# Kernel tuning notes

Hardware: AMD Instinct MI355X
Metric: run time of the kernel (lower is better)

Reference implementation:

```python
import jax, jax.numpy as jnp
import numpy as np

H, KVH, D, HID = 32, 32, 128, 4096
THETA = 10000.0
EPS = 1e-5


def setup_inputs() -> dict:
    key = jax.random.key(0)
    ks = jax.random.split(key, 7)
    T = 2048
    return {
        "positions": jnp.arange(T, dtype=jnp.int32),
        "hidden_states": jax.random.normal(ks[0], (T, HID), dtype=jnp.float32),
        "w_qkv": jax.random.normal(ks[1], ((H + 2 * KVH) * D, HID), dtype=jnp.float32) * 0.02,
        "w_o": jax.random.normal(ks[2], (HID, H * D), dtype=jnp.float32) * 0.02,
        "q_norm_w": jax.random.uniform(ks[3], (H, D), dtype=jnp.float32),
        "q_norm_b": jax.random.normal(ks[4], (H, D), dtype=jnp.float32) * 0.02,
        "k_norm_w": jax.random.uniform(ks[5], (KVH, D), dtype=jnp.float32),
        "k_norm_b": jax.random.normal(ks[6], (KVH, D), dtype=jnp.float32) * 0.02,
    }


def _per_head_ln(x, w, b):
    # x: [T, H, D]; layer_norm over last dim without affine, then *w + b (per head)
    mu = jnp.mean(x, axis=-1, keepdims=True)
    var = jnp.mean(jnp.square(x - mu), axis=-1, keepdims=True)
    xn = (x - mu) * jax.lax.rsqrt(var + EPS)
    return xn * w + b


def _rope(x, positions):
    # neox-style rotate-half RoPE; x: [T, H, D]
    half = D // 2
    inv_freq = 1.0 / (THETA ** (jnp.arange(0, D, 2, dtype=jnp.float32) / D))  # [D/2]
    freqs = positions.astype(jnp.float32)[:, None] * inv_freq  # [T, D/2]
    cos = jnp.cos(freqs)[:, None, :]  # [T, 1, D/2]
    sin = jnp.sin(freqs)[:, None, :]
    x1, x2 = x[..., :half], x[..., half:]
    return jnp.concatenate([x1 * cos - x2 * sin, x2 * cos + x1 * sin], axis=-1)


def reference(positions, hidden_states, w_qkv, w_o, q_norm_w, q_norm_b, k_norm_w, k_norm_b):
    T = hidden_states.shape[0]
    qkv = hidden_states @ w_qkv.T  # [T, (H+2*KVH)*D]
    q, k, v = jnp.split(qkv, [H * D, (H + KVH) * D], axis=-1)
    q = q.reshape(T, H, D)
    k = k.reshape(T, KVH, D)
    v = v.reshape(T, KVH, D)
    q = _per_head_ln(q, q_norm_w, q_norm_b)
    k = _per_head_ln(k, k_norm_w, k_norm_b)
    q = _rope(q, positions)
    k = _rope(k, positions)
    scale = D ** -0.5
    scores = jnp.einsum("qhd,khd->hqk", q, k) * scale  # [H, T, T]
    causal = jnp.tril(jnp.ones((T, T), dtype=bool))
    scores = jnp.where(causal, scores, jnp.finfo(scores.dtype).min)
    probs = jax.nn.softmax(scores, axis=-1)
    attn = jnp.einsum("hqk,khd->qhd", probs, v).reshape(T, H * D)
    return attn @ w_o.T  # [T, HID]
```

## Files before the change

### kernel.cpp

```cpp
#include <hip/hip_runtime.h>
#include <cstdint>

typedef unsigned short u16;
typedef __attribute__((ext_vector_type(8))) __bf16 bf16x8;
typedef __attribute__((ext_vector_type(4))) float f32x4;

__device__ __forceinline__ u16 f2bf(float f) {
  unsigned int u = __builtin_bit_cast(unsigned int, f);
  unsigned int r = (u + 0x7fffu + ((u >> 16) & 1u)) >> 16;
  return (u16)r;
}
__device__ __forceinline__ float bf2f(u16 u) {
  return __builtin_bit_cast(float, (unsigned int)u << 16);
}

__device__ __forceinline__ void gload16(const u16* g, u16* l) {
  __builtin_amdgcn_global_load_lds((const __attribute__((address_space(1))) void*)g,
                                   (__attribute__((address_space(3))) void*)l, 16, 0, 0);
}

__device__ __forceinline__ int swz64i(int row, int col) {
  return row * 64 + (((col & 0x38) ^ ((row & 7) << 3)) | (col & 7));
}
__device__ __forceinline__ int swz128i(int row, int col) {
  return row * 128 + (((col & 0x78) ^ ((row & 7) << 3)) | (col & 7));
}

__global__ __launch_bounds__(256) void cvt_bf16_kernel(const float* __restrict__ in,
                                                       u16* __restrict__ out, long n4) {
  long i = (long)blockIdx.x * 256 + threadIdx.x;
  long stride = (long)gridDim.x * 256;
  const float4* in4 = (const float4*)in;
  uint2* out2 = (uint2*)out;
  for (long k = i; k < n4; k += stride) {
    float4 v = in4[k];
    uint2 o;
    o.x = (unsigned int)f2bf(v.x) | ((unsigned int)f2bf(v.y) << 16);
    o.y = (unsigned int)f2bf(v.z) | ((unsigned int)f2bf(v.w) << 16);
    out2[k] = o;
  }
}

__global__ __launch_bounds__(512, 2) void gemm192(const u16* __restrict__ A,
                                                  const u16* __restrict__ B,
                                                  u16* __restrict__ C,
                                                  int Ndim, int Kdim) {
  extern __shared__ __align__(16) u16 lds[];
  const int tid = threadIdx.x;
  const int lane = tid & 63, wave = tid >> 6;
  const int wr = wave >> 2, wc = wave & 3;
  const int l15 = lane & 15, l4 = lane >> 4;
  const int gx = gridDim.x;
  int lin = blockIdx.y * gx + blockIdx.x;
  const int xcd = lin & 7, ii = lin >> 3;
  const int bx = xcd * (gx >> 3) + (ii >> 3), by = ii & 7;
  const long arow = (long)by * 256, brow = (long)bx * 192;
  const int NT = Kdim >> 6;

  const int rowt = tid >> 3;
  const int koff = ((tid & 7) ^ (rowt & 7)) * 8;
  const u16* gA[4];
  const u16* gB[3];
  #pragma unroll
  for (int r = 0; r < 4; ++r) gA[r] = A + (size_t)(arow + rowt + r * 64) * Kdim + koff;
  #pragma unroll
  for (int r = 0; r < 3; ++r) gB[r] = B + (size_t)(brow + rowt + r * 64) * Kdim + koff;
  u16* const ldsB = lds + 49152;

  auto STA = [&](int u) {
    u16* d = lds + (u % 3) * 16384 + tid * 8;
    #pragma unroll
    for (int r = 0; r < 4; ++r) gload16(gA[r] + (size_t)u * 64, d + r * 4096);
  };
  auto STB = [&](int u) {
    u16* d = ldsB + (u & 1) * 12288 + tid * 8;
    #pragma unroll
    for (int r = 0; r < 3; ++r) gload16(gB[r] + (size_t)u * 64, d + r * 4096);
  };

  bf16x8 af[4][2], bfr[3][2];
  f32x4 acc[8][3] = {};
  int cks[2];
  #pragma unroll
  for (int kc = 0; kc < 2; ++kc) cks[kc] = (((kc * 4 + l4) ^ (l15 & 7)) * 8);

  auto LDA4 = [&](int u, int mh) {
    const u16* base = lds + (u % 3) * 16384 + (wr * 128 + mh * 64 + l15) * 64;
    #pragma unroll
    for (int m = 0; m < 4; ++m)
      #pragma unroll
      for (int kc = 0; kc < 2; ++kc)
        af[m][kc] = *(const bf16x8*)(base + m * 1024 + cks[kc]);
  };
  auto LDBall = [&](int u) {
    const u16* base = ldsB + (u & 1) * 12288 + (wc * 48 + l15) * 64;
    #pragma unroll
    for (int nh = 0; nh < 3; ++nh)
      #pragma unroll
      for (int kc = 0; kc < 2; ++kc)
        bfr[nh][kc] = *(const bf16x8*)(base + nh * 1024 + cks[kc]);
  };
  auto MM24 = [&](int mh) {
    #pragma unroll
    for (int kc = 0; kc < 2; ++kc)
      #pragma unroll
      for (int m = 0; m < 4; ++m)
        #pragma unroll
        for (int nh = 0; nh < 3; ++nh)
          acc[mh * 4 + m][nh] = __builtin_amdgcn_mfma_f32_16x16x32_bf16(
              af[m][kc], bfr[nh][kc], acc[mh * 4 + m][nh], 0, 0, 0);
  };

#define PH_BEGIN() do { __builtin_amdgcn_s_barrier();                         \
    asm volatile("s_waitcnt lgkmcnt(0)" ::: "memory");                        \
    __builtin_amdgcn_sched_barrier(0);                                        \
    __builtin_amdgcn_s_setprio(1); } while (0)
#define PH_END() do { __builtin_amdgcn_s_setprio(0);                          \
    __builtin_amdgcn_s_barrier(); } while (0)

  STA(0); STB(0); STA(1);
  asm volatile("s_waitcnt vmcnt(4)" ::: "memory");
  __builtin_amdgcn_s_barrier();

  for (int u = 0; u < NT; ++u) {
    LDA4(u, 0); LDBall(u);
    if (u + 1 < NT) STB(u + 1);
    PH_BEGIN(); MM24(0); PH_END();
    LDA4(u, 1);
    if (u + 2 < NT) STA(u + 2);
    PH_BEGIN(); MM24(1);
    __builtin_amdgcn_s_setprio(0);
    if (u + 2 < NT) { asm volatile("s_waitcnt vmcnt(4)" ::: "memory"); }
    else            { asm volatile("s_waitcnt vmcnt(0)" ::: "memory"); }
    __builtin_amdgcn_s_barrier();
  }
#undef PH_BEGIN
#undef PH_END

  #pragma unroll
  for (int m = 0; m < 8; ++m)
    #pragma unroll
    for (int nh = 0; nh < 3; ++nh)
      #pragma unroll
      for (int j = 0; j < 4; ++j) {
        long r = arow + wr * 128 + m * 16 + l4 * 4 + j;
        long c = brow + wc * 48 + nh * 16 + l15;
        C[r * Ndim + c] = f2bf(acc[m][nh][j]);
      }
}

__global__ __launch_bounds__(512, 2) void gemm256(const u16* __restrict__ A,
                                                  const u16* __restrict__ B,
                                                  float* __restrict__ C,
                                                  int Ndim, int Kdim) {
  extern __shared__ __align__(16) u16 lds[];
  const int tid = threadIdx.x;
  const int lane = tid & 63, wave = tid >> 6;
  const int wr = wave >> 2, wc = wave & 3;
  const int l15 = lane & 15, l4 = lane >> 4;
  const int gx = gridDim.x;
  int lin = blockIdx.y * gx + blockIdx.x;
  const int xcd = lin & 7, ii = lin >> 3;
  const int bx = xcd * (gx >> 3) + (ii >> 3), by = ii & 7;
  const long arow = (long)by * 256, brow = (long)bx * 128;
  const int NT = Kdim >> 6;

  const int rowt = tid >> 3;
  const int koff = ((tid & 7) ^ (rowt & 7)) * 8;
  const u16* gA[4];
  const u16* gB[2];
  #pragma unroll
  for (int r = 0; r < 4; ++r) gA[r] = A + (size_t)(arow + rowt + r * 64) * Kdim + koff;
  #pragma unroll
  for (int r = 0; r < 2; ++r) gB[r] = B + (size_t)(brow + rowt + r * 64) * Kdim + koff;

  auto STA = [&](int u) {
    u16* d = lds + (u % 3) * 16384 + tid * 8;
    #pragma unroll
    for (int r = 0; r < 4; ++r) gload16(gA[r] + (size_t)u * 64, d + r * 4096);
  };
  auto STB = [&](int u) {
    u16* d = lds + 49152 + (u & 1) * 8192 + tid * 8;
    #pragma unroll
    for (int r = 0; r < 2; ++r) gload16(gB[r] + (size_t)u * 64, d + r * 4096);
  };

  bf16x8 af[4][2], bfr[2][2];
  f32x4 acc[8][2] = {};
  int cks[2];
  #pragma unroll
  for (int kc = 0; kc < 2; ++kc) cks[kc] = (((kc * 4 + l4) ^ (l15 & 7)) * 8);

  auto LDA = [&](int u, int mh) {
    const u16* base = lds + (u % 3) * 16384 + (wr * 128 + mh * 64 + l15) * 64;
    #pragma unroll
    for (int m = 0; m < 4; ++m)
      #pragma unroll
      for (int kc = 0; kc < 2; ++kc)
        af[m][kc] = *(const bf16x8*)(base + m * 1024 + cks[kc]);
  };
  auto LDB = [&](int u) {
    const u16* base = lds + 49152 + (u & 1) * 8192 + (wc * 32 + l15) * 64;
    #pragma unroll
    for (int n = 0; n < 2; ++n)
      #pragma unroll
      for (int kc = 0; kc < 2; ++kc)
        bfr[n][kc] = *(const bf16x8*)(base + n * 1024 + cks[kc]);
  };
  auto MM = [&](int mh) {
    #pragma unroll
    for (int kc = 0; kc < 2; ++kc)
      #pragma unroll
      for (int m = 0; m < 4; ++m)
        #pragma unroll
        for (int n = 0; n < 2; ++n)
          acc[mh * 4 + m][n] =
            __builtin_amdgcn_mfma_f32_16x16x32_bf16(af[m][kc], bfr[n][kc],
                                                    acc[mh * 4 + m][n], 0, 0, 0);
  };

#define PH_BEGIN() do { __builtin_amdgcn_s_barrier();                         \
    asm volatile("s_waitcnt lgkmcnt(0)" ::: "memory");                        \
    __builtin_amdgcn_sched_barrier(0);                                        \
    __builtin_amdgcn_s_setprio(1); } while (0)

  STA(0); STB(0); STA(1); STB(1);
  asm volatile("s_waitcnt vmcnt(6)" ::: "memory");
  __builtin_amdgcn_s_barrier();

  for (int u = 0; u < NT; ++u) {
    LDA(u, 0); LDB(u);
    if (u + 2 < NT) STA(u + 2);
    PH_BEGIN(); MM(0);
    __builtin_amdgcn_s_setprio(0);
    __builtin_amdgcn_s_barrier();
    LDA(u, 1);
    if (u + 2 < NT) STB(u + 2);
    PH_BEGIN(); MM(1);
    __builtin_amdgcn_s_setprio(0);
    if (u + 2 < NT) { asm volatile("s_waitcnt vmcnt(6)" ::: "memory"); }
    else if (u + 1 < NT) { asm volatile("s_waitcnt vmcnt(0)" ::: "memory"); }
    __builtin_amdgcn_s_barrier();
  }
#undef PH_BEGIN

  #pragma unroll
  for (int M = 0; M < 8; ++M)
    #pragma unroll
    for (int n = 0; n < 2; ++n)
      #pragma unroll
      for (int j = 0; j < 4; ++j) {
        long r = arow + wr * 128 + M * 16 + l4 * 4 + j;
        long c = brow + wc * 32 + n * 16 + l15;
        C[r * Ndim + c] = acc[M][n][j];
      }
}

__global__ __launch_bounds__(256) void ln_rope_kernel(
    const u16* __restrict__ qkv, const int* __restrict__ pos,
    const float* __restrict__ qw, const float* __restrict__ qb2,
    const float* __restrict__ kw, const float* __restrict__ kb2,
    u16* __restrict__ qo, u16* __restrict__ ko, u16* __restrict__ vo, int T) {
  const int hh = blockIdx.x;
  const int t = blockIdx.y * 4 + (threadIdx.x >> 6);
  const int lane = threadIdx.x & 63;
  const u16* src = qkv + (size_t)t * 12288 + hh * 128;
  u16 u1 = src[lane], u2 = src[lane + 64];
  if (hh >= 64) {
    u16* dst = vo + ((size_t)(hh - 64) * T + t) * 128;
    dst[lane] = u1; dst[lane + 64] = u2;
    return;
  }
  float x1 = bf2f(u1), x2 = bf2f(u2);
  float s = x1 + x2;
  #pragma unroll
  for (int off = 32; off; off >>= 1) s += __shfl_xor(s, off);
  float mu = s * (1.0f / 128.0f);
  float d1 = x1 - mu, d2 = x2 - mu;
  float vs = d1 * d1 + d2 * d2;
  #pragma unroll
  for (int off = 32; off; off >>= 1) vs += __shfl_xor(vs, off);
  float rstd = rsqrtf(vs * (1.0f / 128.0f) + 1e-5f);
  bool isq = hh < 32;
  int hl = isq ? hh : hh - 32;
  const float* w = (isq ? qw : kw) + hl * 128;
  const float* b = (isq ? qb2 : kb2) + hl * 128;
  float y1 = d1 * rstd * w[lane] + b[lane];
  float y2 = d2 * rstd * w[lane + 64] + b[lane + 64];
  float p = (float)pos[t];
  float invf = exp2f((float)lane * (-13.287712379549449f / 64.0f));
  float fr = p * invf;
  float sn, cs;
  __sincosf(fr, &sn, &cs);
  float o1 = y1 * cs - y2 * sn;
  float o2 = y2 * cs + y1 * sn;
  if (isq) {
    const float sc = 0.08838834764831845f;
    o1 *= sc; o2 *= sc;
    u16* dst = qo + ((size_t)hl * T + t) * 128;
    dst[lane] = f2bf(o1); dst[lane + 64] = f2bf(o2);
  } else {
    u16* dst = ko + ((size_t)hl * T + t) * 128;
    dst[lane] = f2bf(o1); dst[lane + 64] = f2bf(o2);
  }
}

__global__ __launch_bounds__(512, 2) void flash_kernel(
    const u16* __restrict__ qb, const u16* __restrict__ kb,
    const u16* __restrict__ vb, u16* __restrict__ attn, int T) {
  extern __shared__ __align__(16) u16 flds[];
  u16* const Ks = flds;
  u16* const Vt = flds + 8192;
  u16* const Ps = flds + 16384;
  const int tid = threadIdx.x;
  const int lane = tid & 63, wave = tid >> 6;
  const int wl = wave & 3;
  const int l15 = lane & 15, l4 = lane >> 4;
  const int h = blockIdx.y;
  const int nqt = T >> 7;
  const int qt = (wave < 4) ? (nqt - 1 - blockIdx.x) : blockIdx.x;
  const int qbase = qt * 128;
  const u16* Q  = qb + (size_t)h * T * 128;
  const u16* Kp = kb + (size_t)h * T * 128;
  const u16* Vp = vb + (size_t)h * T * 128;
  const int rK = tid >> 4, d8k = (tid & 15) * 8;
  const int rv = tid & 63, dv0 = (tid >> 6) * 8;
  u16* const Pw = Ps + wave * 2048;

  bf16x8 qf[2][4];
  #pragma unroll
  for (int mi = 0; mi < 2; ++mi)
    #pragma unroll
    for (int kc = 0; kc < 4; ++kc)
      qf[mi][kc] = *(const bf16x8*)&Q[(size_t)(qbase + mi * 64 + wl * 16 + l15) * 128 + kc * 32 + l4 * 8];

  float m_st[2][4], l_st[2][4];
  f32x4 o[2][8] = {};
  #pragma unroll
  for (int mi = 0; mi < 2; ++mi)
    #pragma unroll
    for (int j = 0; j < 4; ++j) { m_st[mi][j] = -1e30f; l_st[mi][j] = 0.0f; }

  const int ntile = 2 * (nqt - 1 - blockIdx.x) + 2;
  uint4 kr[2], vr[2];
  #pragma unroll
  for (int c = 0; c < 2; ++c) {
    kr[c] = *(const uint4*)&Kp[(size_t)(rK + 32 * c) * 128 + d8k];
    vr[c] = *(const uint4*)&Vp[(size_t)rv * 128 + dv0 + 64 * c];
  }
  for (int kt = 0; kt < ntile; ++kt) {
    const int kbase = kt * 64;
    #pragma unroll
    for (int c = 0; c < 2; ++c) {
      *(uint4*)&Ks[swz128i(rK + 32 * c, d8k)] = kr[c];
      const u16* pv = (const u16*)&vr[c];
      #pragma unroll
      for (int j = 0; j < 8; ++j) Vt[swz64i(dv0 + 64 * c + j, rv)] = pv[j];
    }
    __syncthreads();
    if (kt + 1 < ntile) {
      const int nb = kbase + 64;
      #pragma unroll
      for (int c = 0; c < 2; ++c) {
        kr[c] = *(const uint4*)&Kp[(size_t)(nb + rK + 32 * c) * 128 + d8k];
        vr[c] = *(const uint4*)&Vp[(size_t)(nb + rv) * 128 + dv0 + 64 * c];
      }
    }
    #pragma unroll
    for (int mi = 0; mi < 2; ++mi) {
      const int r0 = qbase + mi * 64 + wl * 16;
      if (kbase <= r0 + 15) {
        f32x4 s[4] = {};
        __builtin_amdgcn_s_setprio(1);
        #pragma unroll
        for (int kc = 0; kc < 4; ++kc)
          #pragma unroll
          for (int nj = 0; nj < 4; ++nj) {
            bf16x8 kf = *(const bf16x8*)&Ks[swz128i(nj * 16 + l15, kc * 32 + l4 * 8)];
            s[nj] = __builtin_amdgcn_mfma_f32_16x16x32_bf16(qf[mi][kc], kf, s[nj], 0, 0, 0);
          }
        __builtin_amdgcn_s_setprio(0);
        if (kbase + 63 > r0) {
          #pragma unroll
          for (int nj = 0; nj < 4; ++nj)
            #pragma unroll
            for (int j = 0; j < 4; ++j) {
              int r = r0 + l4 * 4 + j;
              int cc = kbase + nj * 16 + l15;
              if (cc > r) s[nj][j] = -1e30f;
            }
        }
        float vmax[4];
        float dmax = -1e30f;
        #pragma unroll
        for (int j = 0; j < 4; ++j) {
          float v = fmaxf(fmaxf(s[0][j], s[1][j]), fmaxf(s[2][j], s[3][j]));
          #pragma unroll
          for (int off = 1; off < 16; off <<= 1) v = fmaxf(v, __shfl_xor(v, off));
          vmax[j] = v;
          dmax = fmaxf(dmax, v - m_st[mi][j]);
        }
        if (!__all(dmax <= 8.0f)) {
          #pragma unroll
          for (int j = 0; j < 4; ++j) {
            float mn = fmaxf(m_st[mi][j], vmax[j]);
            float scl = __expf(m_st[mi][j] - mn);
            m_st[mi][j] = mn;
            l_st[mi][j] *= scl;
            #pragma unroll
            for (int nf = 0; nf < 8; ++nf) o[mi][nf][j] *= scl;
          }
        }
        float sum[4] = {0.f, 0.f, 0.f, 0.f};
        #pragma unroll
        for (int nj = 0; nj < 4; ++nj)
          #pragma unroll
          for (int j = 0; j < 4; ++j) {
            float p = __expf(s[nj][j] - m_st[mi][j]);
            s[nj][j] = p;
            sum[j] += p;
          }
        #pragma unroll
        for (int j = 0; j < 4; ++j) {
          #pragma unroll
          for (int off = 1; off < 16; off <<= 1) sum[j] += __shfl_xor(sum[j], off);
          l_st[mi][j] += sum[j];
        }
        #pragma unroll
        for (int nj = 0; nj < 4; ++nj)
          #pragma unroll
          for (int j = 0; j < 4; ++j)
            Pw[swz64i(mi * 16 + l4 * 4 + j, nj * 16 + l15)] = f2bf(s[nj][j]);
        asm volatile("s_waitcnt lgkmcnt(0)" ::: "memory");
        __builtin_amdgcn_sched_barrier(0);
        __builtin_amdgcn_s_setprio(1);
        #pragma unroll
        for (int kc = 0; kc < 2; ++kc) {
          bf16x8 pf = *(const bf16x8*)&Pw[swz64i(mi * 16 + l15, kc * 32 + l4 * 8)];
          #pragma unroll
          for (int nf = 0; nf < 8; ++nf) {
            bf16x8 vf = *(const bf16x8*)&Vt[swz64i(nf * 16 + l15, kc * 32 + l4 * 8)];
            o[mi][nf] = __builtin_amdgcn_mfma_f32_16x16x32_bf16(pf, vf, o[mi][nf], 0, 0, 0);
          }
        }
        __builtin_amdgcn_s_setprio(0);
      }
    }
    __syncthreads();
  }
  #pragma unroll
  for (int mi = 0; mi < 2; ++mi) {
    float rl[4];
    #pragma unroll
    for (int j = 0; j < 4; ++j) rl[j] = 1.0f / l_st[mi][j];
    #pragma unroll
    for (int nf = 0; nf < 8; ++nf)
      #pragma unroll
      for (int j = 0; j < 4; ++j) {
        int r = qbase + mi * 64 + wl * 16 + l4 * 4 + j;
        int cc = h * 128 + nf * 16 + l15;
        attn[(size_t)r * 4096 + cc] = f2bf(o[mi][nf][j] * rl[j]);
      }
  }
}

extern "C" void kernel_launch(void* const* d_in, const int* in_sizes, int n_in,
                              void* d_out, int out_size, void* d_ws, size_t ws_size,
                              hipStream_t stream) {
  const int* positions = (const int*)d_in[0];
  const float* hidden  = (const float*)d_in[1];
  const float* w_qkv   = (const float*)d_in[2];
  const float* w_o     = (const float*)d_in[3];
  const float* qnw     = (const float*)d_in[4];
  const float* qnb     = (const float*)d_in[5];
  const float* knw     = (const float*)d_in[6];
  const float* knb     = (const float*)d_in[7];
  float* out = (float*)d_out;

  const int T = in_sizes[0];
  const int HID = 4096, NQKV = 12288, H = 32;

  char* ws = (char*)d_ws;
  u16* hid_bf  = (u16*)ws;
  u16* wreg    = (u16*)(ws + (size_t)T * HID * 2);
  u16* qkv_bf  = (u16*)(ws + (size_t)T * HID * 2 + (size_t)NQKV * HID * 2);

  u16* q_bf  = wreg;
  u16* k_bf  = q_bf + (size_t)H * T * 128;
  u16* v_bf  = k_bf + (size_t)H * T * 128;
  u16* at_bf = v_bf + (size_t)H * T * 128;
  u16* wo_bf = at_bf + (size_t)T * 4096;

  hipFuncSetAttribute(reinterpret_cast<const void*>(&gemm192),
                      hipFuncAttributeMaxDynamicSharedMemorySize, 147456);
  hipFuncSetAttribute(reinterpret_cast<const void*>(&gemm256),
                      hipFuncAttributeMaxDynamicSharedMemorySize, 131072);
  hipFuncSetAttribute(reinterpret_cast<const void*>(&flash_kernel),
                      hipFuncAttributeMaxDynamicSharedMemorySize, 65536);

  cvt_bf16_kernel<<<2048, 256, 0, stream>>>(hidden, hid_bf, (long)T * HID / 4);
  cvt_bf16_kernel<<<4096, 256, 0, stream>>>(w_qkv, wreg, (long)NQKV * HID / 4);
  gemm192<<<dim3(NQKV / 192, T / 256), 512, 147456, stream>>>(hid_bf, wreg, qkv_bf, NQKV, HID);
  ln_rope_kernel<<<dim3(96, T / 4), 256, 0, stream>>>(qkv_bf, positions, qnw, qnb, knw, knb,
                                                      q_bf, k_bf, v_bf, T);
  cvt_bf16_kernel<<<2048, 256, 0, stream>>>(w_o, wo_bf, (long)HID * HID / 4);
  flash_kernel<<<dim3(T / 256, H), 512, 65536, stream>>>(q_bf, k_bf, v_bf, at_bf, T);
  gemm256<<<dim3(HID / 128, T / 256), 512, 131072, stream>>>(at_bf, wo_bf, out, HID, HID);
}
```

Before: 498.6 us.

## Fuse fp32 weight conversion into GEMM B-tile loads

New measurement: 547.5 us. 9.8% more time.

```diff
diff --git a/kernel.cpp b/kernel.cpp
--- a/kernel.cpp
+++ b/kernel.cpp
@@ -12,6 +12,12 @@
 }
 __device__ __forceinline__ float bf2f(u16 u) {
   return __builtin_bit_cast(float, (unsigned int)u << 16);
+}
+__device__ __forceinline__ bf16x8 pack8(float4 a, float4 b) {
+  bf16x8 r;
+  r[0] = (__bf16)a.x; r[1] = (__bf16)a.y; r[2] = (__bf16)a.z; r[3] = (__bf16)a.w;
+  r[4] = (__bf16)b.x; r[5] = (__bf16)b.y; r[6] = (__bf16)b.z; r[7] = (__bf16)b.w;
+  return r;
 }
 
 __device__ __forceinline__ void gload16(const u16* g, u16* l) {
@@ -42,7 +48,7 @@
 }
 
 __global__ __launch_bounds__(512, 2) void gemm192(const u16* __restrict__ A,
-                                                  const u16* __restrict__ B,
+                                                  const float* __restrict__ W,
                                                   u16* __restrict__ C,
                                                   int Ndim, int Kdim) {
   extern __shared__ __align__(16) u16 lds[];
@@ -60,11 +66,11 @@
   const int rowt = tid >> 3;
   const int koff = ((tid & 7) ^ (rowt & 7)) * 8;
   const u16* gA[4];
-  const u16* gB[3];
+  const float* gW[3];
   #pragma unroll
   for (int r = 0; r < 4; ++r) gA[r] = A + (size_t)(arow + rowt + r * 64) * Kdim + koff;
   #pragma unroll
-  for (int r = 0; r < 3; ++r) gB[r] = B + (size_t)(brow + rowt + r * 64) * Kdim + koff;
+  for (int r = 0; r < 3; ++r) gW[r] = W + (size_t)(brow + rowt + r * 64) * Kdim + koff;
   u16* const ldsB = lds + 49152;
 
   auto STA = [&](int u) {
@@ -72,10 +78,19 @@
     #pragma unroll
     for (int r = 0; r < 4; ++r) gload16(gA[r] + (size_t)u * 64, d + r * 4096);
   };
-  auto STB = [&](int u) {
+  float4 breg[3][2];
+  auto GLB = [&](int u) {
+    #pragma unroll
+    for (int r = 0; r < 3; ++r) {
+      breg[r][0] = *(const float4*)(gW[r] + (size_t)u * 64);
+      breg[r][1] = *(const float4*)(gW[r] + (size_t)u * 64 + 4);
+    }
+  };
+  auto CVW = [&](int u) {
     u16* d = ldsB + (u & 1) * 12288 + tid * 8;
     #pragma unroll
-    for (int r = 0; r < 3; ++r) gload16(gB[r] + (size_t)u * 64, d + r * 4096);
+    for (int r = 0; r < 3; ++r)
+      *(bf16x8*)(d + r * 4096) = pack8(breg[r][0], breg[r][1]);
   };
 
   bf16x8 af[4][2], bfr[3][2];
@@ -118,20 +133,27 @@
 #define PH_END() do { __builtin_amdgcn_s_setprio(0);                          \
     __builtin_amdgcn_s_barrier(); } while (0)
 
-  STA(0); STB(0); STA(1);
+  GLB(0);
+  __builtin_amdgcn_sched_barrier(0);
+  STA(0); STA(1);
+  asm volatile("s_waitcnt vmcnt(8)" ::: "memory");
+  CVW(0);
   asm volatile("s_waitcnt vmcnt(4)" ::: "memory");
+  asm volatile("s_waitcnt lgkmcnt(0)" ::: "memory");
   __builtin_amdgcn_s_barrier();
 
   for (int u = 0; u < NT; ++u) {
     LDA4(u, 0); LDBall(u);
-    if (u + 1 < NT) STB(u + 1);
+    if (u + 1 < NT) GLB(u + 1);
+    __builtin_amdgcn_sched_barrier(0);
+    if (u + 2 < NT) STA(u + 2);
     PH_BEGIN(); MM24(0); PH_END();
     LDA4(u, 1);
-    if (u + 2 < NT) STA(u + 2);
+    if (u + 2 < NT) { asm volatile("s_waitcnt vmcnt(4)" ::: "memory"); }
+    else            { asm volatile("s_waitcnt vmcnt(0)" ::: "memory"); }
+    if (u + 1 < NT) CVW(u + 1);
     PH_BEGIN(); MM24(1);
     __builtin_amdgcn_s_setprio(0);
-    if (u + 2 < NT) { asm volatile("s_waitcnt vmcnt(4)" ::: "memory"); }
-    else            { asm volatile("s_waitcnt vmcnt(0)" ::: "memory"); }
     __builtin_amdgcn_s_barrier();
   }
 #undef PH_BEGIN
@@ -150,7 +172,7 @@
 }
 
 __global__ __launch_bounds__(512, 2) void gemm256(const u16* __restrict__ A,
-                                                  const u16* __restrict__ B,
+                                                  const float* __restrict__ W,
                                                   float* __restrict__ C,
                                                   int Ndim, int Kdim) {
   extern __shared__ __align__(16) u16 lds[];
@@ -168,21 +190,30 @@
   const int rowt = tid >> 3;
   const int koff = ((tid & 7) ^ (rowt & 7)) * 8;
   const u16* gA[4];
-  const u16* gB[2];
+  const float* gW[2];
   #pragma unroll
   for (int r = 0; r < 4; ++r) gA[r] = A + (size_t)(arow + rowt + r * 64) * Kdim + koff;
   #pragma unroll
-  for (int r = 0; r < 2; ++r) gB[r] = B + (size_t)(brow + rowt + r * 64) * Kdim + koff;
+  for (int r = 0; r < 2; ++r) gW[r] = W + (size_t)(brow + rowt + r * 64) * Kdim + koff;
 
   auto STA = [&](int u) {
     u16* d = lds + (u % 3) * 16384 + tid * 8;
     #pragma unroll
     for (int r = 0; r < 4; ++r) gload16(gA[r] + (size_t)u * 64, d + r * 4096);
   };
-  auto STB = [&](int u) {
+  float4 breg[2][2];
+  auto GLB = [&](int u) {
+    #pragma unroll
+    for (int r = 0; r < 2; ++r) {
+      breg[r][0] = *(const float4*)(gW[r] + (size_t)u * 64);
+      breg[r][1] = *(const float4*)(gW[r] + (size_t)u * 64 + 4);
+    }
+  };
+  auto CVW = [&](int u) {
     u16* d = lds + 49152 + (u & 1) * 8192 + tid * 8;
     #pragma unroll
-    for (int r = 0; r < 2; ++r) gload16(gB[r] + (size_t)u * 64, d + r * 4096);
+    for (int r = 0; r < 2; ++r)
+      *(bf16x8*)(d + r * 4096) = pack8(breg[r][0], breg[r][1]);
   };
 
   bf16x8 af[4][2], bfr[2][2];
@@ -224,22 +255,37 @@
     __builtin_amdgcn_sched_barrier(0);                                        \
     __builtin_amdgcn_s_setprio(1); } while (0)
 
-  STA(0); STB(0); STA(1); STB(1);
-  asm volatile("s_waitcnt vmcnt(6)" ::: "memory");
+  GLB(0);
+  __builtin_amdgcn_sched_barrier(0);
+  STA(0); STA(1);
+  asm volatile("s_waitcnt vmcnt(8)" ::: "memory");
+  CVW(0);
+  GLB(1);
+  asm volatile("s_waitcnt vmcnt(8)" ::: "memory");
+  CVW(1);
+  asm volatile("s_waitcnt vmcnt(4)" ::: "memory");
+  asm volatile("s_waitcnt lgkmcnt(0)" ::: "memory");
   __builtin_amdgcn_s_barrier();
 
   for (int u = 0; u < NT; ++u) {
     LDA(u, 0); LDB(u);
-    if (u + 2 < NT) STA(u + 2);
+    if (u + 2 < NT) {
+      GLB(u + 2);
+      __builtin_amdgcn_sched_barrier(0);
+      STA(u + 2);
+    }
     PH_BEGIN(); MM(0);
     __builtin_amdgcn_s_setprio(0);
     __builtin_amdgcn_s_barrier();
     LDA(u, 1);
-    if (u + 2 < NT) STB(u + 2);
+    if (u + 2 < NT) {
+      asm volatile("s_waitcnt vmcnt(4)" ::: "memory");
+      CVW(u + 2);
+    } else if (u + 1 < NT) {
+      asm volatile("s_waitcnt vmcnt(0)" ::: "memory");
+    }
     PH_BEGIN(); MM(1);
     __builtin_amdgcn_s_setprio(0);
-    if (u + 2 < NT) { asm volatile("s_waitcnt vmcnt(6)" ::: "memory"); }
-    else if (u + 1 < NT) { asm volatile("s_waitcnt vmcnt(0)" ::: "memory"); }
     __builtin_amdgcn_s_barrier();
   }
 #undef PH_BEGIN
@@ -489,7 +535,6 @@
   u16* k_bf  = q_bf + (size_t)H * T * 128;
   u16* v_bf  = k_bf + (size_t)H * T * 128;
   u16* at_bf = v_bf + (size_t)H * T * 128;
-  u16* wo_bf = at_bf + (size_t)T * 4096;
 
   hipFuncSetAttribute(reinterpret_cast<const void*>(&gemm192),
                       hipFuncAttributeMaxDynamicSharedMemorySize, 147456);
@@ -499,11 +544,9 @@
                       hipFuncAttributeMaxDynamicSharedMemorySize, 65536);
 
   cvt_bf16_kernel<<<2048, 256, 0, stream>>>(hidden, hid_bf, (long)T * HID / 4);
-  cvt_bf16_kernel<<<4096, 256, 0, stream>>>(w_qkv, wreg, (long)NQKV * HID / 4);
-  gemm192<<<dim3(NQKV / 192, T / 256), 512, 147456, stream>>>(hid_bf, wreg, qkv_bf, NQKV, HID);
+  gemm192<<<dim3(NQKV / 192, T / 256), 512, 147456, stream>>>(hid_bf, w_qkv, qkv_bf, NQKV, HID);
   ln_rope_kernel<<<dim3(96, T / 4), 256, 0, stream>>>(qkv_bf, positions, qnw, qnb, knw, knb,
                                                       q_bf, k_bf, v_bf, T);
-  cvt_bf16_kernel<<<2048, 256, 0, stream>>>(w_o, wo_bf, (long)HID * HID / 4);
   flash_kernel<<<dim3(T / 256, H), 512, 65536, stream>>>(q_bf, k_bf, v_bf, at_bf, T);
-  gemm256<<<dim3(HID / 128, T / 256), 512, 131072, stream>>>(at_bf, wo_bf, out, HID, HID);
-}
+  gemm256<<<dim3(HID / 128, T / 256), 512, 131072, stream>>>(at_bf, w_o, out, HID, HID);
+}
```

## Restructure flash attention to one 128-row query tile per block, longest-first

Applied to the files above, without the earlier changes.

After: 493.9 us. No clear change (-1.0%).

```diff
diff --git a/kernel.cpp b/kernel.cpp
--- a/kernel.cpp
+++ b/kernel.cpp
@@ -262,45 +262,50 @@
     const float* __restrict__ kw, const float* __restrict__ kb2,
     u16* __restrict__ qo, u16* __restrict__ ko, u16* __restrict__ vo, int T) {
   const int hh = blockIdx.x;
-  const int t = blockIdx.y * 4 + (threadIdx.x >> 6);
+  const int t0 = blockIdx.y * 16 + (threadIdx.x >> 6) * 4;
   const int lane = threadIdx.x & 63;
-  const u16* src = qkv + (size_t)t * 12288 + hh * 128;
-  u16 u1 = src[lane], u2 = src[lane + 64];
   if (hh >= 64) {
-    u16* dst = vo + ((size_t)(hh - 64) * T + t) * 128;
-    dst[lane] = u1; dst[lane + 64] = u2;
+    #pragma unroll
+    for (int i = 0; i < 4; ++i) {
+      int t = t0 + i;
+      const u16* src = qkv + (size_t)t * 12288 + hh * 128;
+      u16* dst = vo + ((size_t)(hh - 64) * T + t) * 128;
+      dst[lane] = src[lane];
+      dst[lane + 64] = src[lane + 64];
+    }
     return;
   }
-  float x1 = bf2f(u1), x2 = bf2f(u2);
-  float s = x1 + x2;
-  #pragma unroll
-  for (int off = 32; off; off >>= 1) s += __shfl_xor(s, off);
-  float mu = s * (1.0f / 128.0f);
-  float d1 = x1 - mu, d2 = x2 - mu;
-  float vs = d1 * d1 + d2 * d2;
-  #pragma unroll
-  for (int off = 32; off; off >>= 1) vs += __shfl_xor(vs, off);
-  float rstd = rsqrtf(vs * (1.0f / 128.0f) + 1e-5f);
   bool isq = hh < 32;
   int hl = isq ? hh : hh - 32;
-  const float* w = (isq ? qw : kw) + hl * 128;
-  const float* b = (isq ? qb2 : kb2) + hl * 128;
-  float y1 = d1 * rstd * w[lane] + b[lane];
-  float y2 = d2 * rstd * w[lane + 64] + b[lane + 64];
-  float p = (float)pos[t];
+  const float* wp = (isq ? qw : kw) + hl * 128;
+  const float* bp = (isq ? qb2 : kb2) + hl * 128;
+  float w1 = wp[lane], w2 = wp[lane + 64];
+  float b1 = bp[lane], b2 = bp[lane + 64];
   float invf = exp2f((float)lane * (-13.287712379549449f / 64.0f));
-  float fr = p * invf;
-  float sn, cs;
-  __sincosf(fr, &sn, &cs);
-  float o1 = y1 * cs - y2 * sn;
-  float o2 = y2 * cs + y1 * sn;
-  if (isq) {
-    const float sc = 0.08838834764831845f;
-    o1 *= sc; o2 *= sc;
-    u16* dst = qo + ((size_t)hl * T + t) * 128;
-    dst[lane] = f2bf(o1); dst[lane + 64] = f2bf(o2);
-  } else {
-    u16* dst = ko + ((size_t)hl * T + t) * 128;
+  u16* obase = (isq ? qo : ko) + (size_t)hl * T * 128;
+  const float sc = isq ? 0.08838834764831845f : 1.0f;
+  #pragma unroll
+  for (int i = 0; i < 4; ++i) {
+    int t = t0 + i;
+    const u16* src = qkv + (size_t)t * 12288 + hh * 128;
+    float x1 = bf2f(src[lane]), x2 = bf2f(src[lane + 64]);
+    float s = x1 + x2;
+    #pragma unroll
+    for (int off = 32; off; off >>= 1) s += __shfl_xor(s, off);
+    float mu = s * (1.0f / 128.0f);
+    float d1 = x1 - mu, d2 = x2 - mu;
+    float vs = d1 * d1 + d2 * d2;
+    #pragma unroll
+    for (int off = 32; off; off >>= 1) vs += __shfl_xor(vs, off);
+    float rstd = rsqrtf(vs * (1.0f / 128.0f) + 1e-5f);
+    float y1 = d1 * rstd * w1 + b1;
+    float y2 = d2 * rstd * w2 + b2;
+    float fr = (float)pos[t] * invf;
+    float sn, cs;
+    __sincosf(fr, &sn, &cs);
+    float o1 = (y1 * cs - y2 * sn) * sc;
+    float o2 = (y2 * cs + y1 * sn) * sc;
+    u16* dst = obase + (size_t)t * 128;
     dst[lane] = f2bf(o1); dst[lane + 64] = f2bf(o2);
   }
 }
@@ -314,34 +319,31 @@
   u16* const Ps = flds + 16384;
   const int tid = threadIdx.x;
   const int lane = tid & 63, wave = tid >> 6;
-  const int wl = wave & 3;
   const int l15 = lane & 15, l4 = lane >> 4;
-  const int h = blockIdx.y;
+  const int bid = blockIdx.x;
   const int nqt = T >> 7;
-  const int qt = (wave < 4) ? (nqt - 1 - blockIdx.x) : blockIdx.x;
+  const int h = bid & 31;
+  const int qt = (bid < 256) ? (nqt - 1 - (bid >> 5)) : ((bid - 256) >> 5);
   const int qbase = qt * 128;
   const u16* Q  = qb + (size_t)h * T * 128;
   const u16* Kp = kb + (size_t)h * T * 128;
   const u16* Vp = vb + (size_t)h * T * 128;
   const int rK = tid >> 4, d8k = (tid & 15) * 8;
   const int rv = tid & 63, dv0 = (tid >> 6) * 8;
-  u16* const Pw = Ps + wave * 2048;
-
-  bf16x8 qf[2][4];
-  #pragma unroll
-  for (int mi = 0; mi < 2; ++mi)
-    #pragma unroll
-    for (int kc = 0; kc < 4; ++kc)
-      qf[mi][kc] = *(const bf16x8*)&Q[(size_t)(qbase + mi * 64 + wl * 16 + l15) * 128 + kc * 32 + l4 * 8];
-
-  float m_st[2][4], l_st[2][4];
-  f32x4 o[2][8] = {};
-  #pragma unroll
-  for (int mi = 0; mi < 2; ++mi)
-    #pragma unroll
-    for (int j = 0; j < 4; ++j) { m_st[mi][j] = -1e30f; l_st[mi][j] = 0.0f; }
-
-  const int ntile = 2 * (nqt - 1 - blockIdx.x) + 2;
+  u16* const Pw = Ps + wave * 1024;
+
+  const int r0g = qbase + wave * 16;
+  bf16x8 qf[4];
+  #pragma unroll
+  for (int kc = 0; kc < 4; ++kc)
+    qf[kc] = *(const bf16x8*)&Q[(size_t)(r0g + l15) * 128 + kc * 32 + l4 * 8];
+
+  float m_st[4], l_st[4];
+  f32x4 o[8] = {};
+  #pragma unroll
+  for (int j = 0; j < 4; ++j) { m_st[j] = -1e30f; l_st[j] = 0.0f; }
+
+  const int ntile = 2 * qt + 2;
   uint4 kr[2], vr[2];
   #pragma unroll
   for (int c = 0; c < 2; ++c) {
@@ -366,102 +368,95 @@
         vr[c] = *(const uint4*)&Vp[(size_t)(nb + rv) * 128 + dv0 + 64 * c];
       }
     }
-    #pragma unroll
-    for (int mi = 0; mi < 2; ++mi) {
-      const int r0 = qbase + mi * 64 + wl * 16;
-      if (kbase <= r0 + 15) {
-        f32x4 s[4] = {};
-        __builtin_amdgcn_s_setprio(1);
-        #pragma unroll
-        for (int kc = 0; kc < 4; ++kc)
-          #pragma unroll
-          for (int nj = 0; nj < 4; ++nj) {
-            bf16x8 kf = *(const bf16x8*)&Ks[swz128i(nj * 16 + l15, kc * 32 + l4 * 8)];
-            s[nj] = __builtin_amdgcn_mfma_f32_16x16x32_bf16(qf[mi][kc], kf, s[nj], 0, 0, 0);
-          }
-        __builtin_amdgcn_s_setprio(0);
-        if (kbase + 63 > r0) {
-          #pragma unroll
-          for (int nj = 0; nj < 4; ++nj)
-            #pragma unroll
-            for (int j = 0; j < 4; ++j) {
-              int r = r0 + l4 * 4 + j;
-              int cc = kbase + nj * 16 + l15;
-              if (cc > r) s[nj][j] = -1e30f;
-            }
+    if (kbase <= r0g + 15) {
+      f32x4 s[4] = {};
+      __builtin_amdgcn_s_setprio(1);
+      #pragma unroll
+      for (int kc = 0; kc < 4; ++kc)
+        #pragma unroll
+        for (int nj = 0; nj < 4; ++nj) {
+          bf16x8 kf = *(const bf16x8*)&Ks[swz128i(nj * 16 + l15, kc * 32 + l4 * 8)];
+          s[nj] = __builtin_amdgcn_mfma_f32_16x16x32_bf16(qf[kc], kf, s[nj], 0, 0, 0);
         }
-        float vmax[4];
-        float dmax = -1e30f;
-        #pragma unroll
-        for (int j = 0; j < 4; ++j) {
-          float v = fmaxf(fmaxf(s[0][j], s[1][j]), fmaxf(s[2][j], s[3][j]));
-          #pragma unroll
-          for (int off = 1; off < 16; off <<= 1) v = fmaxf(v, __shfl_xor(v, off));
-          vmax[j] = v;
-          dmax = fmaxf(dmax, v - m_st[mi][j]);
-        }
-        if (!__all(dmax <= 8.0f)) {
-          #pragma unroll
-          for (int j = 0; j < 4; ++j) {
-            float mn = fmaxf(m_st[mi][j], vmax[j]);
-            float scl = __expf(m_st[mi][j] - mn);
-            m_st[mi][j] = mn;
-            l_st[mi][j] *= scl;
-            #pragma unroll
-            for (int nf = 0; nf < 8; ++nf) o[mi][nf][j] *= scl;
-          }
-        }
-        float sum[4] = {0.f, 0.f, 0.f, 0.f};
+      __builtin_amdgcn_s_setprio(0);
+      if (kbase + 63 > r0g) {
         #pragma unroll
         for (int nj = 0; nj < 4; ++nj)
           #pragma unroll
           for (int j = 0; j < 4; ++j) {
-            float p = __expf(s[nj][j] - m_st[mi][j]);
-            s[nj][j] = p;
-            sum[j] += p;
+            int r = r0g + l4 * 4 + j;
+            int cc = kbase + nj * 16 + l15;
+            if (cc > r) s[nj][j] = -1e30f;
           }
+      }
+      float vmax[4];
+      float dmax = -1e30f;
+      #pragma unroll
+      for (int j = 0; j < 4; ++j) {
+        float v = fmaxf(fmaxf(s[0][j], s[1][j]), fmaxf(s[2][j], s[3][j]));
+        #pragma unroll
+        for (int off = 1; off < 16; off <<= 1) v = fmaxf(v, __shfl_xor(v, off));
+        vmax[j] = v;
+        dmax = fmaxf(dmax, v - m_st[j]);
+      }
+      if (!__all(dmax <= 8.0f)) {
         #pragma unroll
         for (int j = 0; j < 4; ++j) {
+          float mn = fmaxf(m_st[j], vmax[j]);
+          float scl = __expf(m_st[j] - mn);
+          m_st[j] = mn;
+          l_st[j] *= scl;
           #pragma unroll
-          for (int off = 1; off < 16; off <<= 1) sum[j] += __shfl_xor(sum[j], off);
-          l_st[mi][j] += sum[j];
+          for (int nf = 0; nf < 8; ++nf) o[nf][j] *= scl;
         }
-        #pragma unroll
-        for (int nj = 0; nj < 4; ++nj)
-          #pragma unroll
-          for (int j = 0; j < 4; ++j)
-            Pw[swz64i(mi * 16 + l4 * 4 + j, nj * 16 + l15)] = f2bf(s[nj][j]);
-        asm volatile("s_waitcnt lgkmcnt(0)" ::: "memory");
-        __builtin_amdgcn_sched_barrier(0);
-        __builtin_amdgcn_s_setprio(1);
-        #pragma unroll
-        for (int kc = 0; kc < 2; ++kc) {
-          bf16x8 pf = *(const bf16x8*)&Pw[swz64i(mi * 16 + l15, kc * 32 + l4 * 8)];
-          #pragma unroll
-          for (int nf = 0; nf < 8; ++nf) {
-            bf16x8 vf = *(const bf16x8*)&Vt[swz64i(nf * 16 + l15, kc * 32 + l4 * 8)];
-            o[mi][nf] = __builtin_amdgcn_mfma_f32_16x16x32_bf16(pf, vf, o[mi][nf], 0, 0, 0);
-          }
+      }
+      float sum[4] = {0.f, 0.f, 0.f, 0.f};
+      #pragma unroll
+      for (int nj = 0; nj < 4; ++nj)
+        #pragma unroll
+        for (int j = 0; j < 4; ++j) {
+          float p = __expf(s[nj][j] - m_st[j]);
+          s[nj][j] = p;
+          sum[j] += p;
         }
-        __builtin_amdgcn_s_setprio(0);
-      }
+      #pragma unroll
+      for (int j = 0; j < 4; ++j) {
+        #pragma unroll
+        for (int off = 1; off < 16; off <<= 1) sum[j] += __shfl_xor(sum[j], off);
+        l_st[j] += sum[j];
+      }
+      #pragma unroll
+      for (int nj = 0; nj < 4; ++nj)
+        #pragma unroll
+        for (int j = 0; j < 4; ++j)
+          Pw[swz64i(l4 * 4 + j, nj * 16 + l15)] = f2bf(s[nj][j]);
+      asm volatile("s_waitcnt lgkmcnt(0)" ::: "memory");
+      __builtin_amdgcn_sched_barrier(0);
+      __builtin_amdgcn_s_setprio(1);
+      #pragma unroll
+      for (int kc = 0; kc < 2; ++kc) {
+        bf16x8 pf = *(const bf16x8*)&Pw[swz64i(l15, kc * 32 + l4 * 8)];
+        #pragma unroll
+        for (int nf = 0; nf < 8; ++nf) {
+          bf16x8 vf = *(const bf16x8*)&Vt[swz64i(nf * 16 + l15, kc * 32 + l4 * 8)];
+          o[nf] = __builtin_amdgcn_mfma_f32_16x16x32_bf16(pf, vf, o[nf], 0, 0, 0);
+        }
+      }
+      __builtin_amdgcn_s_setprio(0);
     }
     __syncthreads();
   }
-  #pragma unroll
-  for (int mi = 0; mi < 2; ++mi) {
-    float rl[4];
-    #pragma unroll
-    for (int j = 0; j < 4; ++j) rl[j] = 1.0f / l_st[mi][j];
-    #pragma unroll
-    for (int nf = 0; nf < 8; ++nf)
-      #pragma unroll
-      for (int j = 0; j < 4; ++j) {
-        int r = qbase + mi * 64 + wl * 16 + l4 * 4 + j;
-        int cc = h * 128 + nf * 16 + l15;
-        attn[(size_t)r * 4096 + cc] = f2bf(o[mi][nf][j] * rl[j]);
-      }
-  }
+  float rl[4];
+  #pragma unroll
+  for (int j = 0; j < 4; ++j) rl[j] = 1.0f / l_st[j];
+  #pragma unroll
+  for (int nf = 0; nf < 8; ++nf)
+    #pragma unroll
+    for (int j = 0; j < 4; ++j) {
+      int r = r0g + l4 * 4 + j;
+      int cc = h * 128 + nf * 16 + l15;
+      attn[(size_t)r * 4096 + cc] = f2bf(o[nf][j] * rl[j]);
+    }
 }
 
 extern "C" void kernel_launch(void* const* d_in, const int* in_sizes, int n_in,
@@ -496,14 +491,14 @@
   hipFuncSetAttribute(reinterpret_cast<const void*>(&gemm256),
                       hipFuncAttributeMaxDynamicSharedMemorySize, 131072);
   hipFuncSetAttribute(reinterpret_cast<const void*>(&flash_kernel),
-                      hipFuncAttributeMaxDynamicSharedMemorySize, 65536);
+                      hipFuncAttributeMaxDynamicSharedMemorySize, 49152);
 
   cvt_bf16_kernel<<<2048, 256, 0, stream>>>(hidden, hid_bf, (long)T * HID / 4);
   cvt_bf16_kernel<<<4096, 256, 0, stream>>>(w_qkv, wreg, (long)NQKV * HID / 4);
   gemm192<<<dim3(NQKV / 192, T / 256), 512, 147456, stream>>>(hid_bf, wreg, qkv_bf, NQKV, HID);
-  ln_rope_kernel<<<dim3(96, T / 4), 256, 0, stream>>>(qkv_bf, positions, qnw, qnb, knw, knb,
-                                                      q_bf, k_bf, v_bf, T);
+  ln_rope_kernel<<<dim3(96, T / 16), 256, 0, stream>>>(qkv_bf, positions, qnw, qnb, knw, knb,
+                                                       q_bf, k_bf, v_bf, T);
   cvt_bf16_kernel<<<2048, 256, 0, stream>>>(w_o, wo_bf, (long)HID * HID / 4);
-  flash_kernel<<<dim3(T / 256, H), 512, 65536, stream>>>(q_bf, k_bf, v_bf, at_bf, T);
+  flash_kernel<<<512, 512, 49152, stream>>>(q_bf, k_bf, v_bf, at_bf, T);
   gemm256<<<dim3(HID / 128, T / 256), 512, 131072, stream>>>(at_bf, wo_bf, out, HID, HID);
 }
```
